# Kernel optimization log

Measured on AMD Instinct MI355X. Metric: run time of the kernel, lower is better.

The kernel has to match this reference:

```python
import jax, jax.numpy as jnp
import numpy as np

B, N, F_IN, D, NBLOCKS = 16, 1024, 3, 128, 15
EPS = 1e-5


def setup_inputs() -> dict:
    key = jax.random.key(0)
    ks = jax.random.split(key, 8)
    inputs = jax.random.normal(ks[0], (B, N, F_IN), dtype=jnp.float32)
    # Row-normalized random adjacency as the graph operator L (spectral norm <= 1)
    A = jax.random.uniform(ks[1], (B, N, N), dtype=jnp.float32)
    L = A / jnp.sum(A, axis=-1, keepdims=True)
    mask = (jax.random.uniform(ks[2], (B, N, 1)) < 0.8).astype(jnp.float32)
    mask = mask.at[:, 0, :].set(1.0)  # ensure no empty graph
    W1 = jax.random.normal(ks[3], (F_IN, D), dtype=jnp.float32) / np.sqrt(F_IN)
    b1 = jnp.zeros((D,), jnp.float32)
    W_blocks = jax.random.normal(ks[4], (NBLOCKS, D, D), dtype=jnp.float32) / np.sqrt(D)
    b_blocks = jnp.zeros((NBLOCKS, D), jnp.float32)
    gamma_blocks = jnp.ones((NBLOCKS, D), jnp.float32)
    beta_blocks = jnp.zeros((NBLOCKS, D), jnp.float32)
    gamma1 = jnp.ones((D,), jnp.float32)
    beta1 = jnp.zeros((D,), jnp.float32)
    gamma2 = jnp.ones((D,), jnp.float32)
    beta2 = jnp.zeros((D,), jnp.float32)
    W2 = jax.random.normal(ks[5], (D, D), dtype=jnp.float32) / np.sqrt(D)
    b2 = jnp.zeros((D,), jnp.float32)
    return dict(inputs=inputs, L=L, mask=mask, W1=W1, b1=b1,
                W_blocks=W_blocks, b_blocks=b_blocks,
                gamma_blocks=gamma_blocks, beta_blocks=beta_blocks,
                gamma1=gamma1, beta1=beta1, gamma2=gamma2, beta2=beta2,
                W2=W2, b2=b2)


def _graph_bn(x, gamma, beta):
    # BatchNorm over (batch, nodes) per feature channel (training-mode stats)
    mean = jnp.mean(x, axis=(0, 1), keepdims=True)
    var = jnp.var(x, axis=(0, 1), keepdims=True)
    return (x - mean) * jax.lax.rsqrt(var + EPS) * gamma + beta


def reference(inputs, L, mask, W1, b1, W_blocks, b_blocks,
              gamma_blocks, beta_blocks, gamma1, beta1, gamma2, beta2,
              W2, b2):
    # conv1 (GraphConv k=1): per-node linear
    x1 = jnp.einsum('bnf,fd->bnd', inputs, W1) + b1          # [B,N,D]
    x2 = jnp.zeros_like(x1)

    def step(carry, params):
        a, b_prev = carry
        W, bias, g, be = params
        h = jax.nn.elu(_graph_bn(a, g, be))
        h = jnp.einsum('bnm,bmd->bnd', L, h)                 # Laplacian aggregation
        h = jnp.einsum('bnd,de->bne', h, W) + bias           # LapConv transform
        return (b_prev + h, a), None

    (x1, x2), _ = jax.lax.scan(step, (x1, x2),
                               (W_blocks, b_blocks, gamma_blocks, beta_blocks))

    x = jax.nn.elu(_graph_bn(x1, gamma1, beta1) + _graph_bn(x2, gamma2, beta2))
    # Dropout2d is identity in deterministic/eval reference
    x = jnp.einsum('bnd,de->bne', x, W2) + b2                # conv2 (k=1)
    # masked mean pool over nodes: mask [B,N,1] broadcasts over D
    out = jnp.sum(x * mask, axis=1) / jnp.sum(mask, axis=1)  # [B,D]
    return out
```

## Files before the change

kernel.cpp:

```cpp
#include <hip/hip_runtime.h>

typedef float f32x4 __attribute__((ext_vector_type(4)));
typedef __bf16 bf16x8 __attribute__((ext_vector_type(8)));
typedef unsigned int u32x4 __attribute__((ext_vector_type(4)));
typedef unsigned int u32x2 __attribute__((ext_vector_type(2)));
typedef unsigned short u16;

#define DEV __device__ __forceinline__

DEV u16 f2bf(float f) {
    unsigned int x = __float_as_uint(f);
    x += 0x7fffu + ((x >> 16) & 1u);
    return (u16)(x >> 16);
}
DEV unsigned pk2(float a, float b) {
    return (unsigned)f2bf(a) | ((unsigned)f2bf(b) << 16);
}
DEV float elu(float x) { return x > 0.f ? x : expm1f(x); }

DEV void gload16(const u16* g, void* l) {
    __builtin_amdgcn_global_load_lds(
        (const __attribute__((address_space(1))) unsigned int*)g,
        (__attribute__((address_space(3))) unsigned int*)l,
        16, 0, 0);
}

DEV float aload(const float* p) {
    return __hip_atomic_load(p, __ATOMIC_RELAXED, __HIP_MEMORY_SCOPE_AGENT);
}
DEV void astore(float* p, float v) {
    __hip_atomic_store(p, v, __ATOMIC_RELAXED, __HIP_MEMORY_SCOPE_AGENT);
}

DEV void barw(unsigned* ctr, unsigned cnt) {
    asm volatile("s_waitcnt vmcnt(0) lgkmcnt(0)" ::: "memory");
    __syncthreads();
    if (threadIdx.x == 0) {
        unsigned old = __hip_atomic_fetch_add(ctr, 1u, __ATOMIC_RELAXED,
                                              __HIP_MEMORY_SCOPE_AGENT);
        unsigned tgt = old - (old % cnt) + cnt;
        while (__hip_atomic_load(ctr, __ATOMIC_RELAXED,
                                 __HIP_MEMORY_SCOPE_AGENT) < tgt)
            __builtin_amdgcn_s_sleep(4);
    }
    __syncthreads();
}

constexpr float INV_M = 1.f / 16384.f;
constexpr float EPSV  = 1e-5f;

__global__ __launch_bounds__(512) void k_iter(
        int k,
        const float* __restrict__ in, const float* __restrict__ L,
        const float* __restrict__ mask, const float* __restrict__ W1,
        const float* __restrict__ b1, const float* __restrict__ Wb,
        const float* __restrict__ bblk, const float* __restrict__ gb,
        const float* __restrict__ beb, const float* __restrict__ g1,
        const float* __restrict__ be1, const float* __restrict__ g2,
        const float* __restrict__ be2, const float* __restrict__ W2,
        const float* __restrict__ b2,
        u16* __restrict__ Lb, u16* __restrict__ WT,
        float* __restrict__ xA, float* __restrict__ xB,
        u16* __restrict__ hT, float* __restrict__ SP0, float* __restrict__ SP1,
        unsigned* __restrict__ bar, float* __restrict__ poolP,
        float* __restrict__ maskP, float* __restrict__ out) {
    extern __shared__ char smem[];
    int t = threadIdx.x;
    int bid = blockIdx.x;
    int wg = ((bid & 7) << 5) | (bid >> 3);
    int bb = wg >> 4, n0 = (wg & 15) << 6;
    int l = t & 63, w = t >> 6;
    int wm = w >> 2, wn = w & 3;
    int l16 = l & 15, ld16 = l >> 4;

    float* xcur = (k & 1) ? xB : xA;
    float* spa = (k & 1) ? SP1 : SP0;
    float* spz = (k & 1) ? SP0 : SP1;

    if (k == 0) {
        for (long v = (long)bid * 512 + t; v < 2097152; v += 131072) {
            long i = v * 8;
            f32x4 a = *(const f32x4*)(L + i);
            f32x4 b = *(const f32x4*)(L + i + 4);
            u32x4 pv;
            pv[0] = pk2(a[0], a[1]); pv[1] = pk2(a[2], a[3]);
            pv[2] = pk2(b[0], b[1]); pv[3] = pk2(b[2], b[3]);
            *(u32x4*)(Lb + i) = pv;
        }
        for (int o = bid * 512 + t; o < 245760; o += 131072) {
            int kk = o >> 14, r = o & 16383, e = r >> 7, d = r & 127;
            WT[o] = f2bf(Wb[(kk << 14) + (d << 7) + e]);
        }
        float* red0 = (float*)smem;
        float* red1 = (float*)(smem + 8192);
        int c4 = (t & 31) * 4, rg = t >> 5;
        float w0[4], w1v[4], w2v[4], bb4[4];
#pragma unroll
        for (int c = 0; c < 4; ++c) {
            w0[c] = W1[c4 + c]; w1v[c] = W1[128 + c4 + c];
            w2v[c] = W1[256 + c4 + c]; bb4[c] = b1[c4 + c];
        }
        float s[4] = {}, q[4] = {};
        long R = (long)wg * 64;
#pragma unroll
        for (int i = 0; i < 4; ++i) {
            long grow = R + rg + 16 * i;
            float f0 = in[grow * 3], f1 = in[grow * 3 + 1], f2 = in[grow * 3 + 2];
            f32x4 v, z = {0.f, 0.f, 0.f, 0.f};
#pragma unroll
            for (int c = 0; c < 4; ++c) {
                float val = f0 * w0[c] + f1 * w1v[c] + f2 * w2v[c] + bb4[c];
                v[c] = val; s[c] += val; q[c] += val * val;
            }
            *(f32x4*)(xA + grow * 128 + c4) = v;
            *(f32x4*)(xB + grow * 128 + c4) = z;
        }
#pragma unroll
        for (int c = 0; c < 4; ++c) {
            red0[rg * 128 + c4 + c] = s[c]; red1[rg * 128 + c4 + c] = q[c];
        }
        __syncthreads();
        if (t < 128) {
            float a = 0;
#pragma unroll
            for (int g = 0; g < 16; ++g) a += red0[g * 128 + t];
            atomicAdd(&SP0[bb * 256 + t], a);
        } else if (t < 256) {
            int c = t - 128; float a = 0;
#pragma unroll
            for (int g = 0; g < 16; ++g) a += red1[g * 128 + c];
            atomicAdd(&SP0[bb * 256 + 128 + c], a);
        }
        __builtin_amdgcn_fence(__ATOMIC_RELEASE, "agent");
        barw(bar, 256);
    } else {
        u16* As = (u16*)smem;
        u16* Bs = (u16*)(smem + 24576);
        float* red = (float*)(smem + 73728);
        const u16* gA = Lb + ((long)(bb * 1024 + n0)) * 1024;
        const u16* gB = hT + (long)bb * 131072;

        if (k <= 14 && (wg & 15) == 0 && t < 256) astore(&spz[bb * 256 + t], 0.f);

#define STAGE(buf, kt_) do {                                                  \
        int k0_ = (kt_) * 64;                                                 \
        { int u = t; int r = u >> 3, sl = u & 7;                              \
          gload16(gA + (long)r * 1024 + k0_ + ((sl ^ (r & 7)) << 3),          \
                  (char*)As + (buf) * 8192 + u * 16); }                       \
        _Pragma("unroll")                                                     \
        for (int j = 0; j < 2; ++j) {                                         \
            int u = t + 512 * j; int r = u >> 3, sl = u & 7;                  \
            gload16(gB + (long)r * 1024 + k0_ + ((sl ^ (r & 7)) << 3),        \
                    (char*)Bs + (buf) * 16384 + u * 16);                      \
        }                                                                     \
    } while (0)

        f32x4 acc[2][2] = {};
        STAGE(0, 0);
        STAGE(1, 1);
        asm volatile("s_waitcnt vmcnt(3)" ::: "memory");
        __builtin_amdgcn_s_barrier();

        for (int kt = 0; kt < 16; ++kt) {
            if (kt <= 13) STAGE((kt + 2) % 3, kt + 2);
            const char* Ab = (const char*)As + (kt % 3) * 8192;
            const char* Bb = (const char*)Bs + (kt % 3) * 16384;
            __builtin_amdgcn_s_setprio(1);
#pragma unroll
            for (int ks = 0; ks < 2; ++ks) {
                int kb = ks * 64 + ld16 * 16;
                bf16x8 af[2], bfr[2];
#pragma unroll
                for (int m = 0; m < 2; ++m) {
                    int r = wm * 32 + m * 16 + l16;
                    af[m] = *(const bf16x8*)(Ab + r * 128 + (kb ^ ((r & 7) << 4)));
                }
#pragma unroll
                for (int n = 0; n < 2; ++n) {
                    int e = wn * 32 + n * 16 + l16;
                    bfr[n] = *(const bf16x8*)(Bb + e * 128 + (kb ^ ((e & 7) << 4)));
                }
#pragma unroll
                for (int m = 0; m < 2; ++m)
#pragma unroll
                    for (int n = 0; n < 2; ++n)
                        acc[m][n] = __builtin_amdgcn_mfma_f32_16x16x32_bf16(
                            af[m], bfr[n], acc[m][n], 0, 0, 0);
            }
            __builtin_amdgcn_s_setprio(0);
            if (kt <= 13) {
                asm volatile("s_waitcnt vmcnt(3)" ::: "memory");
                __builtin_amdgcn_s_barrier();
            } else if (kt == 14) {
                asm volatile("s_waitcnt vmcnt(0)" ::: "memory");
                __builtin_amdgcn_s_barrier();
            }
        }
#undef STAGE

        float* dst = xcur + (long)wg * 8192;
        const float* biasv = bblk + (k - 1) * 128;
#pragma unroll
        for (int n = 0; n < 2; ++n) {
            int e = wn * 32 + n * 16 + l16;
            float bv = biasv[e];
            float sv = 0.f, qv = 0.f;
#pragma unroll
            for (int m = 0; m < 2; ++m) {
                int row0 = wm * 32 + m * 16 + ld16 * 4;
                float* dp = dst + (long)row0 * 128 + e;
#pragma unroll
                for (int j = 0; j < 4; ++j) {
                    float v = dp[j * 128] + acc[m][n][j] + bv;
                    dp[j * 128] = v;
                    sv += v; qv += v * v;
                }
            }
            red[(wm * 4 + ld16) * 128 + e] = sv;
            red[(8 + wm * 4 + ld16) * 128 + e] = qv;
        }
        __syncthreads();
        if (t < 128) {
            float a = 0;
#pragma unroll
            for (int g = 0; g < 8; ++g) a += red[g * 128 + t];
            atomicAdd(&spa[bb * 256 + t], a);
        } else if (t < 256) {
            int c = t - 128; float a = 0;
#pragma unroll
            for (int g = 0; g < 8; ++g) a += red[(8 + g) * 128 + c];
            atomicAdd(&spa[bb * 256 + 128 + c], a);
        }
        barw(bar, 256);
    }

    if (k < 15) {
        u16* Ws = (u16*)smem;
        u16* Hs = (u16*)(smem + 32768);
        float* st = (float*)(smem + 49152);
        float* sc = (float*)(smem + 50176);
        float* sh = (float*)(smem + 50688);
        if (t < 256) {
            float s = 0.f;
#pragma unroll
            for (int i = 0; i < 16; ++i) s += aload(&spa[i * 256 + t]);
            st[t] = s;
        }
        const u32x4* wsrc = (const u32x4*)(WT + (size_t)k * 16384);
#pragma unroll
        for (int i = 0; i < 4; ++i) {
            int u = t + 512 * i;
            int r = u >> 4, sl = u & 15;
            *(u32x4*)((char*)Ws + r * 256 + ((sl ^ (r & 7)) << 4)) = wsrc[u];
        }
        __syncthreads();
        if (t < 128) {
            float mean = st[t] * INV_M, var = st[128 + t] * INV_M - mean * mean;
            float a = rsqrtf(var + EPSV) * gb[k * 128 + t];
            sc[t] = a; sh[t] = beb[k * 128 + t] - mean * a;
        }
        __syncthreads();
        const float* xb = xcur + (long)wg * 8192;
#pragma unroll
        for (int i = 0; i < 4; ++i) {
            int idx = t + 512 * i;
            int row = idx >> 5, c4 = (idx & 31) * 4;
            f32x4 v = *(const f32x4*)(xb + row * 128 + c4);
            float h0 = elu(v[0] * sc[c4]     + sh[c4]);
            float h1 = elu(v[1] * sc[c4 + 1] + sh[c4 + 1]);
            float h2 = elu(v[2] * sc[c4 + 2] + sh[c4 + 2]);
            float h3 = elu(v[3] * sc[c4 + 3] + sh[c4 + 3]);
            u32x2 pw = {pk2(h0, h1), pk2(h2, h3)};
            *(u32x2*)((char*)Hs + row * 256 + ((c4 * 2) ^ ((row & 7) << 4))) = pw;
        }
        __syncthreads();
        f32x4 acc[2][2] = {};
#pragma unroll
        for (int ks = 0; ks < 4; ++ks) {
            int kb = ks * 64 + ld16 * 16;
            bf16x8 af[2], bfr[2];
#pragma unroll
            for (int m = 0; m < 2; ++m) {
                int r = wm * 32 + m * 16 + l16;
                af[m] = *(const bf16x8*)((char*)Hs + r * 256 + (kb ^ ((r & 7) << 4)));
            }
#pragma unroll
            for (int n = 0; n < 2; ++n) {
                int e = wn * 32 + n * 16 + l16;
                bfr[n] = *(const bf16x8*)((char*)Ws + e * 256 + (kb ^ ((e & 7) << 4)));
            }
#pragma unroll
            for (int m = 0; m < 2; ++m)
#pragma unroll
                for (int n = 0; n < 2; ++n)
                    acc[m][n] = __builtin_amdgcn_mfma_f32_16x16x32_bf16(
                        af[m], bfr[n], acc[m][n], 0, 0, 0);
        }
        __syncthreads();
#pragma unroll
        for (int m = 0; m < 2; ++m)
#pragma unroll
            for (int n = 0; n < 2; ++n) {
                int e = wn * 32 + n * 16 + l16;
                int row0 = wm * 32 + m * 16 + ld16 * 4;
                u32x2 pw = {pk2(acc[m][n][0], acc[m][n][1]),
                            pk2(acc[m][n][2], acc[m][n][3])};
                *(u32x2*)((char*)Hs + e * 128 + ((row0 * 2) ^ ((e & 7) << 4))) = pw;
            }
        __syncthreads();
        {
            int e = t >> 2, sg = t & 3;
            const char* base = (const char*)Hs + e * 128;
            u16* orow = hT + ((long)(bb * 128 + e)) * 1024 + n0 + sg * 16;
#pragma unroll
            for (int u = 0; u < 2; ++u) {
                u32x4 v = *(const u32x4*)(base + ((sg * 32 + u * 16) ^ ((e & 7) << 4)));
                *(u32x4*)(orow + u * 8) = v;
            }
        }
    } else {
        float* x1p = xcur;
        float* x2p = (k & 1) ? xA : xB;
        float* sc1 = (float*)smem;
        float* sh1 = sc1 + 128;
        float* sc2 = sh1 + 128;
        float* sh2 = sc2 + 128;
        float* msk = (float*)(smem + 2048);
        float* fred = (float*)(smem + 4096);
        if (t < 256) {
            int which = t >> 7, c = t & 127;
            const float* p = which ? SP0 : SP1;
            float s = 0.f, q = 0.f;
#pragma unroll
            for (int i = 0; i < 16; ++i) {
                s += aload(&p[i * 256 + c]); q += aload(&p[i * 256 + 128 + c]);
            }
            float mean = s * INV_M, var = q * INV_M - mean * mean;
            float a = rsqrtf(var + EPSV) * (which ? g2[c] : g1[c]);
            (which ? sc2 : sc1)[c] = a;
            (which ? sh2 : sh1)[c] = (which ? be2[c] : be1[c]) - mean * a;
        } else if (t < 320) {
            msk[t - 256] = mask[bb * 1024 + n0 + (t - 256)];
        }
        __syncthreads();
        const float* xb1 = x1p + (long)wg * 8192;
        const float* xb2 = x2p + (long)wg * 8192;
        int row0 = t >> 5, c = (t & 31) * 4;
        f32x4 accv = {0.f, 0.f, 0.f, 0.f};
#pragma unroll
        for (int i = 0; i < 4; ++i) {
            int row = row0 + 16 * i;
            f32x4 v1 = *(const f32x4*)(xb1 + row * 128 + c);
            f32x4 v2 = *(const f32x4*)(xb2 + row * 128 + c);
            float m = msk[row];
            accv[0] += elu(v1[0]*sc1[c]   + sh1[c]   + v2[0]*sc2[c]   + sh2[c])   * m;
            accv[1] += elu(v1[1]*sc1[c+1] + sh1[c+1] + v2[1]*sc2[c+1] + sh2[c+1]) * m;
            accv[2] += elu(v1[2]*sc1[c+2] + sh1[c+2] + v2[2]*sc2[c+2] + sh2[c+2]) * m;
            accv[3] += elu(v1[3]*sc1[c+3] + sh1[c+3] + v2[3]*sc2[c+3] + sh2[c+3]) * m;
        }
        fred[row0 * 128 + c]     = accv[0];
        fred[row0 * 128 + c + 1] = accv[1];
        fred[row0 * 128 + c + 2] = accv[2];
        fred[row0 * 128 + c + 3] = accv[3];
        __syncthreads();
        if (t < 128) {
            float s = 0;
#pragma unroll
            for (int g = 0; g < 16; ++g) s += fred[g * 128 + t];
            astore(&poolP[wg * 128 + t], s);
        }
        if (t == 128) {
            float sm = 0;
#pragma unroll
            for (int j = 0; j < 64; ++j) sm += msk[j];
            astore(&maskP[wg], sm);
        }
        barw(bar, 256);
        if (wg < 16) {
            float* pooled = (float*)smem;
            __syncthreads();
            if (t < 128) {
                float s = 0.f;
                for (int tl = 0; tl < 16; ++tl)
                    s += aload(&poolP[(wg * 16 + tl) * 128 + t]);
                pooled[t] = s;
            }
            if (t == 128) {
                float sm = 0.f;
                for (int tl = 0; tl < 16; ++tl) sm += aload(&maskP[wg * 16 + tl]);
                pooled[128] = 1.f / sm;
            }
            __syncthreads();
            if (t < 128) {
                float acc = 0.f, inv = pooled[128];
                for (int d = 0; d < 128; ++d) acc += pooled[d] * W2[d * 128 + t];
                out[wg * 128 + t] = acc * inv + b2[t];
            }
        }
    }
}


extern "C" void kernel_launch(void* const* d_in, const int* in_sizes, int n_in,
                              void* d_out, int out_size, void* d_ws, size_t ws_size,
                              hipStream_t stream) {
    const float* inputs = (const float*)d_in[0];
    const float* L      = (const float*)d_in[1];
    const float* mask   = (const float*)d_in[2];
    const float* W1     = (const float*)d_in[3];
    const float* b1     = (const float*)d_in[4];
    const float* Wb     = (const float*)d_in[5];
    const float* bblk   = (const float*)d_in[6];
    const float* gb     = (const float*)d_in[7];
    const float* beb    = (const float*)d_in[8];
    const float* g1     = (const float*)d_in[9];
    const float* be1    = (const float*)d_in[10];
    const float* g2     = (const float*)d_in[11];
    const float* be2    = (const float*)d_in[12];
    const float* W2     = (const float*)d_in[13];
    const float* b2     = (const float*)d_in[14];
    float* out = (float*)d_out;

    char* ws = (char*)d_ws;
    u16*      Lb    = (u16*)(ws);
    u16*      WT    = (u16*)(ws + 33554432);
    float*    xA    = (float*)(ws + 34045952);
    float*    xB    = (float*)(ws + 42434560);
    u16*      hT    = (u16*)(ws + 50823168);
    float*    poolP = (float*)(ws + 50823168);
    float*    maskP = (float*)(ws + 50823168 + 131072);
    float*    SP0   = (float*)(ws + 55017472);
    float*    SP1   = (float*)(ws + 55017472 + 16384);
    unsigned* bar   = (unsigned*)(ws + 55017472 + 32768);

    hipMemsetAsync(ws + 55017472, 0, 32768 + 1024, stream);

    for (int k = 0; k <= 15; ++k) {
        hipLaunchKernelGGL(k_iter, dim3(256), dim3(512), 81920, stream, k,
                           inputs, L, mask, W1, b1, Wb, bblk, gb, beb,
                           g1, be1, g2, be2, W2, b2,
                           Lb, WT, xA, xB, hT, SP0, SP1, bar, poolP, maskP, out);
    }
}
```

Baseline: 414.1 us.

## Split one-time prep into wide kernel and deepen GEMM pipeline to four stages

```diff
diff --git a/kernel.cpp b/kernel.cpp
--- a/kernel.cpp
+++ b/kernel.cpp
@@ -49,17 +49,82 @@
 constexpr float INV_M = 1.f / 16384.f;
 constexpr float EPSV  = 1e-5f;
 
+__global__ __launch_bounds__(256) void k_prep(
+        const float* __restrict__ in, const float* __restrict__ L,
+        const float* __restrict__ W1, const float* __restrict__ b1,
+        const float* __restrict__ Wb,
+        u16* __restrict__ Lb, u16* __restrict__ WT,
+        float* __restrict__ xA, float* __restrict__ xB,
+        float* __restrict__ SP0) {
+    int t = threadIdx.x, bid = blockIdx.x;
+    {
+        long base = (long)bid * 1024;
+#pragma unroll
+        for (int j = 0; j < 4; ++j) {
+            long i = (base + j * 256 + t) * 8;
+            f32x4 a = *(const f32x4*)(L + i);
+            f32x4 b = *(const f32x4*)(L + i + 4);
+            u32x4 v;
+            v[0] = pk2(a[0], a[1]); v[1] = pk2(a[2], a[3]);
+            v[2] = pk2(b[0], b[1]); v[3] = pk2(b[2], b[3]);
+            *(u32x4*)(Lb + i) = v;
+        }
+    }
+    if (bid < 960) {
+        int o = bid * 256 + t;
+        int kk = o >> 14, r = o & 16383, e = r >> 7, d = r & 127;
+        WT[o] = f2bf(Wb[(kk << 14) + (d << 7) + e]);
+    }
+    if (bid >= 1024 && bid < 1280) {
+        __shared__ float red[2][8][128];
+        int ib = bid - 1024;
+        long R = (long)ib * 64;
+        int c4 = (t & 31) * 4, rg = t >> 5;
+        float w0[4], w1v[4], w2v[4], bb4[4];
+#pragma unroll
+        for (int c = 0; c < 4; ++c) {
+            w0[c] = W1[c4 + c]; w1v[c] = W1[128 + c4 + c];
+            w2v[c] = W1[256 + c4 + c]; bb4[c] = b1[c4 + c];
+        }
+        float s[4] = {}, q[4] = {};
+#pragma unroll
+        for (int i = 0; i < 8; ++i) {
+            long grow = R + rg + 8 * i;
+            float f0 = in[grow * 3], f1 = in[grow * 3 + 1], f2 = in[grow * 3 + 2];
+            f32x4 v, z = {0.f, 0.f, 0.f, 0.f};
+#pragma unroll
+            for (int c = 0; c < 4; ++c) {
+                float val = f0 * w0[c] + f1 * w1v[c] + f2 * w2v[c] + bb4[c];
+                v[c] = val; s[c] += val; q[c] += val * val;
+            }
+            *(f32x4*)(xA + grow * 128 + c4) = v;
+            *(f32x4*)(xB + grow * 128 + c4) = z;
+        }
+#pragma unroll
+        for (int c = 0; c < 4; ++c) { red[0][rg][c4 + c] = s[c]; red[1][rg][c4 + c] = q[c]; }
+        __syncthreads();
+        if (t < 128) {
+            float a = 0;
+#pragma unroll
+            for (int g = 0; g < 8; ++g) a += red[0][g][t];
+            atomicAdd(&SP0[(ib & 15) * 256 + t], a);
+        } else {
+            int c = t - 128; float a = 0;
+#pragma unroll
+            for (int g = 0; g < 8; ++g) a += red[1][g][c];
+            atomicAdd(&SP0[(ib & 15) * 256 + 128 + c], a);
+        }
+    }
+}
+
 __global__ __launch_bounds__(512) void k_iter(
         int k,
-        const float* __restrict__ in, const float* __restrict__ L,
-        const float* __restrict__ mask, const float* __restrict__ W1,
-        const float* __restrict__ b1, const float* __restrict__ Wb,
-        const float* __restrict__ bblk, const float* __restrict__ gb,
-        const float* __restrict__ beb, const float* __restrict__ g1,
-        const float* __restrict__ be1, const float* __restrict__ g2,
-        const float* __restrict__ be2, const float* __restrict__ W2,
-        const float* __restrict__ b2,
-        u16* __restrict__ Lb, u16* __restrict__ WT,
+        const float* __restrict__ mask, const float* __restrict__ bblk,
+        const float* __restrict__ gb, const float* __restrict__ beb,
+        const float* __restrict__ g1, const float* __restrict__ be1,
+        const float* __restrict__ g2, const float* __restrict__ be2,
+        const float* __restrict__ W2, const float* __restrict__ b2,
+        const u16* __restrict__ Lb, const u16* __restrict__ WT,
         float* __restrict__ xA, float* __restrict__ xB,
         u16* __restrict__ hT, float* __restrict__ SP0, float* __restrict__ SP1,
         unsigned* __restrict__ bar, float* __restrict__ poolP,
@@ -77,66 +142,10 @@
     float* spa = (k & 1) ? SP1 : SP0;
     float* spz = (k & 1) ? SP0 : SP1;
 
-    if (k == 0) {
-        for (long v = (long)bid * 512 + t; v < 2097152; v += 131072) {
-            long i = v * 8;
-            f32x4 a = *(const f32x4*)(L + i);
-            f32x4 b = *(const f32x4*)(L + i + 4);
-            u32x4 pv;
-            pv[0] = pk2(a[0], a[1]); pv[1] = pk2(a[2], a[3]);
-            pv[2] = pk2(b[0], b[1]); pv[3] = pk2(b[2], b[3]);
-            *(u32x4*)(Lb + i) = pv;
-        }
-        for (int o = bid * 512 + t; o < 245760; o += 131072) {
-            int kk = o >> 14, r = o & 16383, e = r >> 7, d = r & 127;
-            WT[o] = f2bf(Wb[(kk << 14) + (d << 7) + e]);
-        }
-        float* red0 = (float*)smem;
-        float* red1 = (float*)(smem + 8192);
-        int c4 = (t & 31) * 4, rg = t >> 5;
-        float w0[4], w1v[4], w2v[4], bb4[4];
-#pragma unroll
-        for (int c = 0; c < 4; ++c) {
-            w0[c] = W1[c4 + c]; w1v[c] = W1[128 + c4 + c];
-            w2v[c] = W1[256 + c4 + c]; bb4[c] = b1[c4 + c];
-        }
-        float s[4] = {}, q[4] = {};
-        long R = (long)wg * 64;
-#pragma unroll
-        for (int i = 0; i < 4; ++i) {
-            long grow = R + rg + 16 * i;
-            float f0 = in[grow * 3], f1 = in[grow * 3 + 1], f2 = in[grow * 3 + 2];
-            f32x4 v, z = {0.f, 0.f, 0.f, 0.f};
-#pragma unroll
-            for (int c = 0; c < 4; ++c) {
-                float val = f0 * w0[c] + f1 * w1v[c] + f2 * w2v[c] + bb4[c];
-                v[c] = val; s[c] += val; q[c] += val * val;
-            }
-            *(f32x4*)(xA + grow * 128 + c4) = v;
-            *(f32x4*)(xB + grow * 128 + c4) = z;
-        }
-#pragma unroll
-        for (int c = 0; c < 4; ++c) {
-            red0[rg * 128 + c4 + c] = s[c]; red1[rg * 128 + c4 + c] = q[c];
-        }
-        __syncthreads();
-        if (t < 128) {
-            float a = 0;
-#pragma unroll
-            for (int g = 0; g < 16; ++g) a += red0[g * 128 + t];
-            atomicAdd(&SP0[bb * 256 + t], a);
-        } else if (t < 256) {
-            int c = t - 128; float a = 0;
-#pragma unroll
-            for (int g = 0; g < 16; ++g) a += red1[g * 128 + c];
-            atomicAdd(&SP0[bb * 256 + 128 + c], a);
-        }
-        __builtin_amdgcn_fence(__ATOMIC_RELEASE, "agent");
-        barw(bar, 256);
-    } else {
+    if (k > 0) {
         u16* As = (u16*)smem;
-        u16* Bs = (u16*)(smem + 24576);
-        float* red = (float*)(smem + 73728);
+        u16* Bs = (u16*)(smem + 32768);
+        float* red = (float*)smem;
         const u16* gA = Lb + ((long)(bb * 1024 + n0)) * 1024;
         const u16* gB = hT + (long)bb * 131072;
 
@@ -158,13 +167,14 @@
         f32x4 acc[2][2] = {};
         STAGE(0, 0);
         STAGE(1, 1);
-        asm volatile("s_waitcnt vmcnt(3)" ::: "memory");
+        STAGE(2, 2);
+        asm volatile("s_waitcnt vmcnt(6)" ::: "memory");
         __builtin_amdgcn_s_barrier();
 
         for (int kt = 0; kt < 16; ++kt) {
-            if (kt <= 13) STAGE((kt + 2) % 3, kt + 2);
-            const char* Ab = (const char*)As + (kt % 3) * 8192;
-            const char* Bb = (const char*)Bs + (kt % 3) * 16384;
+            if (kt <= 12) STAGE((kt + 3) & 3, kt + 3);
+            const char* Ab = (const char*)As + (kt & 3) * 8192;
+            const char* Bb = (const char*)Bs + (kt & 3) * 16384;
             __builtin_amdgcn_s_setprio(1);
 #pragma unroll
             for (int ks = 0; ks < 2; ++ks) {
@@ -188,7 +198,10 @@
                             af[m], bfr[n], acc[m][n], 0, 0, 0);
             }
             __builtin_amdgcn_s_setprio(0);
-            if (kt <= 13) {
+            if (kt <= 12) {
+                asm volatile("s_waitcnt vmcnt(6)" ::: "memory");
+                __builtin_amdgcn_s_barrier();
+            } else if (kt == 13) {
                 asm volatile("s_waitcnt vmcnt(3)" ::: "memory");
                 __builtin_amdgcn_s_barrier();
             } else if (kt == 14) {
@@ -435,10 +448,12 @@
 
     hipMemsetAsync(ws + 55017472, 0, 32768 + 1024, stream);
 
+    hipLaunchKernelGGL(k_prep, dim3(2048), dim3(256), 0, stream,
+                       inputs, L, W1, b1, Wb, Lb, WT, xA, xB, SP0);
+
     for (int k = 0; k <= 15; ++k) {
-        hipLaunchKernelGGL(k_iter, dim3(256), dim3(512), 81920, stream, k,
-                           inputs, L, mask, W1, b1, Wb, bblk, gb, beb,
-                           g1, be1, g2, be2, W2, b2,
+        hipLaunchKernelGGL(k_iter, dim3(256), dim3(512), 98304, stream, k,
+                           mask, bblk, gb, beb, g1, be1, g2, be2, W2, b2,
                            Lb, WT, xA, xB, hT, SP0, SP1, bar, poolP, maskP, out);
     }
 }
```

New measurement: 356.2 us. 1.16x faster.
